# Kernel optimization log

Measured on AMD Instinct MI355X. Metric: run time of the kernel, lower is better.

Reference implementation:

```python
import jax, jax.numpy as jnp
import numpy as np

B, N_ATOM, N_TOK = 1, 1536, 384
C_ATOM, C_PAIR, C_TOK = 128, 16, 384
C_HID, H, L = 32, 4, 3
HID = 2 * C_ATOM  # n_transition = 2
N_QUERY, N_KEY, INF = 32, 128, 1e9


def _ln(x, gamma=None, beta=None, eps=1e-5):
    mu = jnp.mean(x, axis=-1, keepdims=True)
    var = jnp.mean(jnp.square(x - mu), axis=-1, keepdims=True)
    y = (x - mu) * jax.lax.rsqrt(var + eps)
    if gamma is not None:
        y = y * gamma
    if beta is not None:
        y = y + beta
    return y


def _adaln(a, s, gamma_s, Wg, bg, Ws):
    an = _ln(a)            # LN without affine
    sn = _ln(s, gamma_s)   # scale-only LN
    return jax.nn.sigmoid(sn @ Wg + bg) * an + sn @ Ws


def _block_mask():
    # AtomTransformer.forward: 32-query x 128-key block-local mask
    offset = N_QUERY // 2 - 0.5
    n_center = N_ATOM // N_QUERY + 1
    centers = offset + jnp.arange(n_center, dtype=jnp.float32) * N_QUERY
    idx = jnp.arange(N_ATOM, dtype=jnp.float32)[:, None]
    row = (jnp.abs(idx - centers[None, :]) < N_QUERY / 2).astype(jnp.float32)
    col = (jnp.abs(idx - centers[None, :]) < N_KEY / 2).astype(jnp.float32)
    return (row @ col.T - 1.0) * INF   # [N,N]: 0 in-window, -INF outside


def _forward(ref_pos, ref_mask, ref_element, ref_charge, ref_atom_name_chars,
             ref_space_uid, token_mask, atom_to_token_index,
             W_feats, W_ref_offset, W_inv_sq, W_valid, W_l, W_m,
             W_mlp1, W_mlp2, W_mlp3, W_out_tok,
             attn_ada_gamma_s, attn_ada_Wg, attn_ada_bg, attn_ada_Ws,
             Wq, bq, Wk, Wv, lnz_g, lnz_b, Wb, Wgate, Wo, Wsg, bsg,
             tr_ada_gamma_s, tr_ada_Wg, tr_ada_bg, tr_ada_Ws,
             tr_W1, tr_W2, tr_Wog, tr_bog, tr_Wout):
    # --- RefAtomFeatureEmbedder (AF3 Alg 5 lines 1-6) ---
    feats = jnp.concatenate([
        ref_pos, ref_mask[..., None], ref_element, ref_charge[..., None],
        ref_atom_name_chars.reshape(B, N_ATOM, -1), ref_space_uid[..., None]], axis=-1)
    cl = feats @ W_feats                                     # [B,N,C_ATOM]
    d = ref_pos[:, None, :, :] - ref_pos[:, :, None, :]      # d[l,m] = pos[m]-pos[l]
    v = (ref_space_uid[:, None, :] == ref_space_uid[:, :, None]).astype(jnp.float32)[..., None]
    plm = (d @ W_ref_offset) * v
    inv_sq = 1.0 / (1.0 + jnp.sum(d * d, axis=-1, keepdims=True))
    plm = plm + (inv_sq @ W_inv_sq) * v + (v @ W_valid) * v  # [B,N,N,C_PAIR]
    ql = cl
    # --- single -> pair conditioning + pair MLP ---
    crelu = jax.nn.relu(cl)
    plm = plm + (crelu @ W_l)[:, :, None, :] + (crelu @ W_m)[:, None, :, :]
    h = jax.nn.relu(plm) @ W_mlp1
    h = jax.nn.relu(h) @ W_mlp2
    h = jax.nn.relu(h) @ W_mlp3
    plm = plm + h
    # --- AtomTransformer (Alg 7) -> DiffusionTransformer (Alg 23) ---
    beta = _block_mask()                                     # [N,N]
    atom_mask = jnp.einsum('blt,bt->bl', atom_to_token_index, token_mask)
    mask_bias = (atom_mask - 1.0)[:, None, None, :] * INF    # [B,1,1,N]
    a, s = ql, cl
    inv_sqrt = 1.0 / np.sqrt(C_HID)
    for i in range(L):
        # AttentionPairBias (Alg 24)
        an = _adaln(a, s, attn_ada_gamma_s[i], attn_ada_Wg[i], attn_ada_bg[i], attn_ada_Ws[i])
        q = (an @ Wq[i] + bq[i]).reshape(B, N_ATOM, H, C_HID)
        k = (an @ Wk[i]).reshape(B, N_ATOM, H, C_HID)
        vv = (an @ Wv[i]).reshape(B, N_ATOM, H, C_HID)
        zb = _ln(plm, lnz_g[i], lnz_b[i]) @ Wb[i]            # [B,N,N,H]
        logits = (jnp.einsum('bqhc,bkhc->bhqk', q, k) * inv_sqrt
                  + jnp.moveaxis(zb, -1, 1) + beta[None, None] + mask_bias)
        A = jax.nn.softmax(logits, axis=-1)
        o = jnp.einsum('bhqk,bkhc->bqhc', A, vv)
        g = jax.nn.sigmoid(an @ Wgate[i]).reshape(B, N_ATOM, H, C_HID)
        o = (g * o).reshape(B, N_ATOM, H * C_HID) @ Wo[i]
        attn_out = jax.nn.sigmoid(s @ Wsg[i] + bsg[i]) * o
        # ConditionedTransitionBlock (Alg 25) on pre-attention a (Alg 23)
        tn = _adaln(a, s, tr_ada_gamma_s[i], tr_ada_Wg[i], tr_ada_bg[i], tr_ada_Ws[i])
        hh = jax.nn.silu(tn @ tr_W1[i]) * (tn @ tr_W2[i])
        tr_out = jax.nn.sigmoid(s @ tr_Wog[i] + tr_bog[i]) * (hh @ tr_Wout[i])
        a = attn_out + tr_out
    # --- mean-aggregate atoms -> tokens (Alg 5 line 15) ---
    al = jax.nn.relu(a @ W_out_tok)                          # [B,N,C_TOK]
    counts = jnp.maximum(jnp.sum(atom_to_token_index, axis=1), 1.0)
    a_tok = jnp.einsum('blt,blc->btc', atom_to_token_index, al) / counts[..., None]
    return a_tok


def setup_inputs() -> dict:
    key = jax.random.key(0)
    ks = iter(jax.random.split(key, 80))

    def nrm(shape, scale=0.02):
        return jax.random.normal(next(ks), shape, dtype=jnp.float32) * scale

    inp = {}
    inp['ref_pos'] = jax.random.normal(next(ks), (B, N_ATOM, 3), dtype=jnp.float32) * 3.0
    inp['ref_mask'] = jnp.ones((B, N_ATOM), jnp.float32)
    elem = jax.random.randint(next(ks), (B, N_ATOM), 0, 128)
    inp['ref_element'] = jax.nn.one_hot(elem, 128, dtype=jnp.float32)
    inp['ref_charge'] = jax.random.normal(next(ks), (B, N_ATOM), dtype=jnp.float32)
    chars = jax.random.randint(next(ks), (B, N_ATOM, 4), 0, 64)
    inp['ref_atom_name_chars'] = jax.nn.one_hot(chars, 64, dtype=jnp.float32)
    inp['ref_space_uid'] = jnp.broadcast_to(
        (jnp.arange(N_ATOM) // 8).astype(jnp.float32), (B, N_ATOM))
    inp['token_mask'] = jnp.ones((B, N_TOK), jnp.float32)
    tok = (jnp.arange(N_ATOM) * N_TOK) // N_ATOM  # ~4 atoms per token
    inp['atom_to_token_index'] = jnp.broadcast_to(
        jax.nn.one_hot(tok, N_TOK, dtype=jnp.float32), (B, N_ATOM, N_TOK))
    # embedder params
    inp['W_feats'] = nrm((390, C_ATOM))
    inp['W_ref_offset'] = nrm((3, C_PAIR))
    inp['W_inv_sq'] = nrm((1, C_PAIR))
    inp['W_valid'] = nrm((1, C_PAIR))
    inp['W_l'] = nrm((C_ATOM, C_PAIR))
    inp['W_m'] = nrm((C_ATOM, C_PAIR))
    inp['W_mlp1'] = nrm((C_PAIR, C_PAIR))
    inp['W_mlp2'] = nrm((C_PAIR, C_PAIR))
    inp['W_mlp3'] = nrm((C_PAIR, C_PAIR))
    inp['W_out_tok'] = nrm((C_ATOM, C_TOK))
    # DiffusionTransformer params, stacked over L blocks
    inp['attn_ada_gamma_s'] = jnp.ones((L, C_ATOM), jnp.float32)
    inp['attn_ada_Wg'] = nrm((L, C_ATOM, C_ATOM))
    inp['attn_ada_bg'] = jnp.zeros((L, C_ATOM), jnp.float32)
    inp['attn_ada_Ws'] = nrm((L, C_ATOM, C_ATOM))
    inp['Wq'] = nrm((L, C_ATOM, H * C_HID))
    inp['bq'] = jnp.zeros((L, H * C_HID), jnp.float32)
    inp['Wk'] = nrm((L, C_ATOM, H * C_HID))
    inp['Wv'] = nrm((L, C_ATOM, H * C_HID))
    inp['lnz_g'] = jnp.ones((L, C_PAIR), jnp.float32)
    inp['lnz_b'] = jnp.zeros((L, C_PAIR), jnp.float32)
    inp['Wb'] = nrm((L, C_PAIR, H))
    inp['Wgate'] = nrm((L, C_ATOM, H * C_HID))
    inp['Wo'] = nrm((L, H * C_HID, C_ATOM))
    inp['Wsg'] = nrm((L, C_ATOM, C_ATOM))
    inp['bsg'] = jnp.full((L, C_ATOM), -2.0, jnp.float32)
    inp['tr_ada_gamma_s'] = jnp.ones((L, C_ATOM), jnp.float32)
    inp['tr_ada_Wg'] = nrm((L, C_ATOM, C_ATOM))
    inp['tr_ada_bg'] = jnp.zeros((L, C_ATOM), jnp.float32)
    inp['tr_ada_Ws'] = nrm((L, C_ATOM, C_ATOM))
    inp['tr_W1'] = nrm((L, C_ATOM, HID))
    inp['tr_W2'] = nrm((L, C_ATOM, HID))
    inp['tr_Wog'] = nrm((L, C_ATOM, C_ATOM))
    inp['tr_bog'] = jnp.full((L, C_ATOM), -2.0, jnp.float32)
    inp['tr_Wout'] = nrm((L, HID, C_ATOM))
    return inp


def reference(ref_pos, ref_mask, ref_element, ref_charge, ref_atom_name_chars,
              ref_space_uid, token_mask, atom_to_token_index,
              W_feats, W_ref_offset, W_inv_sq, W_valid, W_l, W_m,
              W_mlp1, W_mlp2, W_mlp3, W_out_tok,
              attn_ada_gamma_s, attn_ada_Wg, attn_ada_bg, attn_ada_Ws,
              Wq, bq, Wk, Wv, lnz_g, lnz_b, Wb, Wgate, Wo, Wsg, bsg,
              tr_ada_gamma_s, tr_ada_Wg, tr_ada_bg, tr_ada_Ws,
              tr_W1, tr_W2, tr_Wog, tr_bog, tr_Wout):
    return _forward(ref_pos, ref_mask, ref_element, ref_charge, ref_atom_name_chars,
                    ref_space_uid, token_mask, atom_to_token_index,
                    W_feats, W_ref_offset, W_inv_sq, W_valid, W_l, W_m,
                    W_mlp1, W_mlp2, W_mlp3, W_out_tok,
                    attn_ada_gamma_s, attn_ada_Wg, attn_ada_bg, attn_ada_Ws,
                    Wq, bq, Wk, Wv, lnz_g, lnz_b, Wb, Wgate, Wo, Wsg, bsg,
                    tr_ada_gamma_s, tr_ada_Wg, tr_ada_bg, tr_ada_Ws,
                    tr_W1, tr_W2, tr_Wog, tr_bog, tr_Wout)
```

## Files before the change

### kernel.cpp

```cpp
#include <hip/hip_runtime.h>
#include <math.h>

#define N_ATOM 1536
#define NB     48
#define NLAYER 3
#define NC     196608L
#define ZSTRIDE 786432L

struct GD { const float* A; const float* B; float* C; const float* ks; const float* bias;
            int act; int ldb; int ldc; int _pad; };
struct GB { GD g[18]; };

__global__ __launch_bounds__(128) void embed_tok_kernel(
    const float* __restrict__ pos, const float* __restrict__ rmask,
    const float* __restrict__ elem, const float* __restrict__ charge,
    const float* __restrict__ chars, const float* __restrict__ uid,
    const float* __restrict__ Wf, const float* __restrict__ W_l, const float* __restrict__ W_m,
    const float* __restrict__ a2t, const float* __restrict__ tmask,
    float* __restrict__ cl, float* __restrict__ aa, float* __restrict__ clnorm,
    float* __restrict__ pl, float* __restrict__ pm,
    int* __restrict__ tok, float* __restrict__ counts, float* __restrict__ amask)
{
  int l = blockIdx.x, c = threadIdx.x;
  __shared__ int sidx[6];
  __shared__ float red[128];
  __shared__ float crow[128];
  if (elem[(long)l * 128 + c] > 0.5f) sidx[0] = c;
  float v0 = chars[(long)l * 256 + c];
  if (v0 > 0.5f) sidx[1 + (c >> 6)] = c & 63;
  float v1 = chars[(long)l * 256 + 128 + c];
  if (v1 > 0.5f) sidx[3 + (c >> 6)] = c & 63;
  for (int j = c; j < 384; j += 128)
    if (a2t[(long)l * 384 + j] > 0.5f) sidx[5] = j;
  __syncthreads();
  float acc = pos[l * 3 + 0] * Wf[c]
            + pos[l * 3 + 1] * Wf[128 + c]
            + pos[l * 3 + 2] * Wf[256 + c]
            + rmask[l] * Wf[384 + c]
            + Wf[(4 + sidx[0]) * 128 + c]
            + charge[l] * Wf[132 * 128 + c]
            + Wf[(133 + sidx[1]) * 128 + c]
            + Wf[(197 + sidx[2]) * 128 + c]
            + Wf[(261 + sidx[3]) * 128 + c]
            + Wf[(325 + sidx[4]) * 128 + c]
            + uid[l] * Wf[389 * 128 + c];
  long gi = (long)l * 128 + c;
  cl[gi] = acc; aa[gi] = acc; crow[c] = fmaxf(acc, 0.f);
  red[c] = acc; __syncthreads();
  for (int s = 64; s > 0; s >>= 1) { if (c < s) red[c] += red[c + s]; __syncthreads(); }
  float mu = red[0] * (1.f / 128.f); __syncthreads();
  float d = acc - mu; red[c] = d * d; __syncthreads();
  for (int s = 64; s > 0; s >>= 1) { if (c < s) red[c] += red[c + s]; __syncthreads(); }
  clnorm[gi] = d * rsqrtf(red[0] * (1.f / 128.f) + 1e-5f);
  if (c < 32) {
    const float* W = (c < 16) ? W_l : W_m;
    int o = c & 15;
    float s = 0.f;
    for (int cc = 0; cc < 128; cc++) s = fmaf(crow[cc], W[cc * 16 + o], s);
    if (c < 16) pl[l * 16 + o] = s; else pm[l * 16 + o] = s;
  }
  if (c == 127) {
    int j = sidx[5];
    tok[l] = j; amask[l] = tmask[j];
    atomicAdd(counts + j, 1.0f);
  }
}

__global__ __launch_bounds__(128) void adaln_kernel(
    const float* __restrict__ a,
    const float* __restrict__ sgA, const float* __restrict__ adA,
    const float* __restrict__ sgT, const float* __restrict__ adT,
    float* __restrict__ an, float* __restrict__ tn)
{
  __shared__ float red[128];
  int l = blockIdx.x, c = threadIdx.x;
  float x = a[(long)l * 128 + c];
  red[c] = x; __syncthreads();
  for (int s = 64; s > 0; s >>= 1) { if (c < s) red[c] += red[c + s]; __syncthreads(); }
  float mu = red[0] * (1.f / 128.f); __syncthreads();
  float d = x - mu; red[c] = d * d; __syncthreads();
  for (int s = 64; s > 0; s >>= 1) { if (c < s) red[c] += red[c + s]; __syncthreads(); }
  float nv = d * rsqrtf(red[0] * (1.f / 128.f) + 1e-5f);
  long i = (long)l * 128 + c;
  an[i] = sgA[i] * nv + adA[i];
  tn[i] = sgT[i] * nv + adT[i];
}

__device__ __forceinline__ void gemm64_body(float* sm, const float* A, const float* B, float* C,
                                            const float* ks, const float* bias, int act,
                                            int ldb, int ldc, int row0, int col0) {
  float* As = sm; float* Bs = sm + 2176;
  int tid = threadIdx.x;
  int tx = tid & 15, ty = tid >> 4;
  float acc[4][4] = {};
  for (int k0 = 0; k0 < 128; k0 += 32) {
    __syncthreads();
    { int r = tid >> 3, k4 = tid & 7;
#pragma unroll
      for (int half = 0; half < 2; half++) {
        int row = r + half * 32;
        float4 v = *(const float4*)(A + (long)(row0 + row) * 128 + k0 + k4 * 4);
        if (ks) { const float* kp = ks + k0 + k4 * 4; v.x *= kp[0]; v.y *= kp[1]; v.z *= kp[2]; v.w *= kp[3]; }
        As[(k4 * 4 + 0) * 68 + row] = v.x; As[(k4 * 4 + 1) * 68 + row] = v.y;
        As[(k4 * 4 + 2) * 68 + row] = v.z; As[(k4 * 4 + 3) * 68 + row] = v.w;
      } }
    { int kk = tid >> 4, n4 = tid & 15;
#pragma unroll
      for (int half = 0; half < 2; half++) {
        int k = kk + half * 16;
        *(float4*)&Bs[k * 68 + n4 * 4] = *(const float4*)(B + (long)(k0 + k) * ldb + col0 + n4 * 4);
      } }
    __syncthreads();
#pragma unroll
    for (int kk = 0; kk < 32; kk++) {
      float4 a = *(const float4*)&As[kk * 68 + ty * 4];
      float4 b = *(const float4*)&Bs[kk * 68 + tx * 4];
      float av[4] = {a.x, a.y, a.z, a.w}, bv[4] = {b.x, b.y, b.z, b.w};
#pragma unroll
      for (int i = 0; i < 4; i++)
#pragma unroll
        for (int j = 0; j < 4; j++) acc[i][j] = fmaf(av[i], bv[j], acc[i][j]);
    }
  }
  __syncthreads();
#pragma unroll
  for (int i = 0; i < 4; i++) {
    int row = row0 + ty * 4 + i;
#pragma unroll
    for (int j = 0; j < 4; j++) {
      int col = col0 + tx * 4 + j;
      float x = acc[i][j];
      if (bias) x += bias[col];
      if (act == 1) x = 1.f / (1.f + expf(-x));
      else if (act == 2) x = fmaxf(x, 0.f);
      C[(long)row * ldc + col] = x;
    }
  }
}

__global__ __launch_bounds__(256) void gemm64(GB args, int M)
{
  __shared__ float sm[4352];
  GD d = args.g[blockIdx.z];
  gemm64_body(sm, d.A, d.B, d.C, d.ks, d.bias, d.act, d.ldb, d.ldc, blockIdx.y * 64, blockIdx.x * 64);
}

__global__ __launch_bounds__(256) void zpre_kernel(
    const float* __restrict__ pos, const float* __restrict__ uid,
    const float* __restrict__ Wro, const float* __restrict__ Winv, const float* __restrict__ Wval,
    const float* __restrict__ M1, const float* __restrict__ M2, const float* __restrict__ M3,
    const float* __restrict__ Lg, const float* __restrict__ Lb, const float* __restrict__ Wb,
    const float* __restrict__ pl, const float* __restrict__ pm, float* __restrict__ zb,
    GB ba)
{
  __shared__ float sm[4352];
  int bid = blockIdx.x, tid = threadIdx.x;
  if (bid >= 768) {
    int u = bid - 768;
    GD d = ba.g[u / 48];
    int tt = u % 48;
    gemm64_body(sm, d.A, d.B, d.C, d.ks, d.bias, d.act, d.ldb, d.ldc, (tt >> 1) * 64, (tt & 1) * 64);
    return;
  }
  if (tid < 48)  sm[tid] = Wro[tid];
  if (tid < 16)  { sm[48 + tid] = Winv[tid]; sm[64 + tid] = Wval[tid]; }
  sm[80 + tid] = M1[tid]; sm[336 + tid] = M2[tid]; sm[592 + tid] = M3[tid];
  if (tid < 48)  { sm[848 + tid] = Lg[tid]; sm[896 + tid] = Lb[tid]; }
  if (tid < 192) sm[944 + tid] = Wb[tid];
  __syncthreads();
  const float* sWro = sm;      const float* sWinv = sm + 48;  const float* sWval = sm + 64;
  const float* sM1 = sm + 80;  const float* sM2 = sm + 336;   const float* sM3 = sm + 592;
  const float* sLg = sm + 848; const float* sLb = sm + 896;   const float* sWb = sm + 944;
  int b = bid >> 4;
  int pc = (bid & 15) * 256 + tid;
  int qi = pc >> 7, kj = pc & 127;
  int l = b * 32 + qi, m = b * 32 - 48 + kj;
  long base = ((long)(b * 32 + qi) * 128 + kj) * 4;
  if (m < 0 || m >= N_ATOM) {
    for (int i = 0; i < NLAYER; i++)
      for (int h = 0; h < 4; h++) zb[i * ZSTRIDE + base + h] = 0.f;
    return;
  }
  float dx = pos[m * 3 + 0] - pos[l * 3 + 0];
  float dy = pos[m * 3 + 1] - pos[l * 3 + 1];
  float dz = pos[m * 3 + 2] - pos[l * 3 + 2];
  float v = (uid[m] == uid[l]) ? 1.f : 0.f;
  float inv = 1.f / (1.f + dx * dx + dy * dy + dz * dz);
  float pv[16], ha[16], hb[16];
#pragma unroll
  for (int j = 0; j < 16; j++)
    pv[j] = v * (dx * sWro[j] + dy * sWro[16 + j] + dz * sWro[32 + j] + inv * sWinv[j] + sWval[j])
            + pl[l * 16 + j] + pm[m * 16 + j];
#pragma unroll
  for (int jo = 0; jo < 16; jo++) { float s = 0.f; for (int ji = 0; ji < 16; ji++) s = fmaf(fmaxf(pv[ji], 0.f), sM1[ji * 16 + jo], s); ha[jo] = s; }
#pragma unroll
  for (int jo = 0; jo < 16; jo++) { float s = 0.f; for (int ji = 0; ji < 16; ji++) s = fmaf(fmaxf(ha[ji], 0.f), sM2[ji * 16 + jo], s); hb[jo] = s; }
#pragma unroll
  for (int jo = 0; jo < 16; jo++) { float s = 0.f; for (int ji = 0; ji < 16; ji++) s = fmaf(fmaxf(hb[ji], 0.f), sM3[ji * 16 + jo], s); ha[jo] = s; }
#pragma unroll
  for (int j = 0; j < 16; j++) pv[j] += ha[j];
  for (int i = 0; i < NLAYER; i++) {
    float mu = 0.f;
#pragma unroll
    for (int j = 0; j < 16; j++) mu += pv[j];
    mu *= (1.f / 16.f);
    float var = 0.f;
#pragma unroll
    for (int j = 0; j < 16; j++) { float dd = pv[j] - mu; var += dd * dd; }
    var *= (1.f / 16.f);
    float rs = rsqrtf(var + 1e-5f);
    float zn[16];
#pragma unroll
    for (int j = 0; j < 16; j++) zn[j] = (pv[j] - mu) * rs * sLg[i * 16 + j] + sLb[i * 16 + j];
    for (int h = 0; h < 4; h++) {
      float s = 0.f;
#pragma unroll
      for (int j = 0; j < 16; j++) s = fmaf(zn[j], sWb[i * 64 + j * 4 + h], s);
      zb[i * ZSTRIDE + base + h] = s;
    }
  }
}

__global__ __launch_bounds__(256) void attn_kernel(
    const float* __restrict__ qb, const float* __restrict__ kb, const float* __restrict__ vb,
    const float* __restrict__ gb, const float* __restrict__ zb, const float* __restrict__ amask,
    float* __restrict__ go)
{
  __shared__ float qs[16][36], ks[128][36], vs[128][36], ps[16][132];
  int bx = blockIdx.x, h = blockIdx.y, t = threadIdx.x;
  int b = bx >> 1, half = bx & 1;
  int q0 = b * 32 + half * 16;
  int kbase = b * 32 - 48;
  if (t < 128) {
    int qi = t >> 3, c4 = t & 7;
    *(float4*)&qs[qi][c4 * 4] = *(const float4*)(qb + (long)(q0 + qi) * 128 + h * 32 + c4 * 4);
  }
  for (int idx = t; idx < 128 * 8; idx += 256) {
    int kj = idx >> 3, c4 = idx & 7;
    int m = kbase + kj;
    float4 kv = make_float4(0.f, 0.f, 0.f, 0.f), vv = make_float4(0.f, 0.f, 0.f, 0.f);
    if (m >= 0 && m < N_ATOM) {
      kv = *(const float4*)(kb + (long)m * 128 + h * 32 + c4 * 4);
      vv = *(const float4*)(vb + (long)m * 128 + h * 32 + c4 * 4);
    }
    *(float4*)&ks[kj][c4 * 4] = kv;
    *(float4*)&vs[kj][c4 * 4] = vv;
  }
  __syncthreads();
  const float isq = 0.17677669529663687f;
  for (int p = t; p < 2048; p += 256) {
    int qi = p >> 7, kj = p & 127;
    int m = kbase + kj;
    float s = 0.f;
#pragma unroll
    for (int c4 = 0; c4 < 8; c4++) {
      float4 a = *(const float4*)&qs[qi][c4 * 4];
      float4 k4 = *(const float4*)&ks[kj][c4 * 4];
      s = fmaf(a.x, k4.x, s); s = fmaf(a.y, k4.y, s);
      s = fmaf(a.z, k4.z, s); s = fmaf(a.w, k4.w, s);
    }
    float logit;
    if (m >= 0 && m < N_ATOM) {
      logit = s * isq + zb[(((long)(q0 + qi)) * 128 + kj) * 4 + h] + (amask[m] - 1.f) * 1e9f;
    } else {
      logit = -1e9f;
    }
    ps[qi][kj] = logit;
  }
  __syncthreads();
  {
    int row = t >> 4, ln = t & 15;
    float mx = -1e30f;
    for (int kj = ln; kj < 128; kj += 16) mx = fmaxf(mx, ps[row][kj]);
#pragma unroll
    for (int o = 8; o > 0; o >>= 1) mx = fmaxf(mx, __shfl_xor(mx, o));
    float sm = 0.f;
    for (int kj = ln; kj < 128; kj += 16) { float e = expf(ps[row][kj] - mx); ps[row][kj] = e; sm += e; }
#pragma unroll
    for (int o = 8; o > 0; o >>= 1) sm += __shfl_xor(sm, o);
    float r = 1.f / sm;
    for (int kj = ln; kj < 128; kj += 16) ps[row][kj] *= r;
  }
  __syncthreads();
  {
    int qi = t >> 4, seg = (t >> 3) & 1, c4 = t & 7;
    float4 acc = make_float4(0.f, 0.f, 0.f, 0.f);
    int kj0 = seg * 64;
#pragma unroll 4
    for (int kj = kj0; kj < kj0 + 64; kj++) {
      float p = ps[qi][kj];
      float4 v = *(const float4*)&vs[kj][c4 * 4];
      acc.x = fmaf(p, v.x, acc.x); acc.y = fmaf(p, v.y, acc.y);
      acc.z = fmaf(p, v.z, acc.z); acc.w = fmaf(p, v.w, acc.w);
    }
    acc.x += __shfl_xor(acc.x, 8);
    acc.y += __shfl_xor(acc.y, 8);
    acc.z += __shfl_xor(acc.z, 8);
    acc.w += __shfl_xor(acc.w, 8);
    if (seg == 0) {
      long gi = (long)(q0 + qi) * 128 + h * 32 + c4 * 4;
      float4 g = *(const float4*)(gb + gi);
      acc.x *= g.x; acc.y *= g.y; acc.z *= g.z; acc.w *= g.w;
      *(float4*)(go + gi) = acc;
    }
  }
}

__global__ __launch_bounds__(256) void gemm_dual32(
    const float* __restrict__ A1, const float* __restrict__ B1,
    const float* __restrict__ h1, const float* __restrict__ h2, const float* __restrict__ B2,
    const float* __restrict__ g1, const float* __restrict__ g2,
    float* __restrict__ C)
{
  __shared__ float As[32 * 36];
  __shared__ float Bs[32 * 68];
  const int N = 128;
  int t = threadIdx.x;
  int row0 = blockIdx.y * 32, col0 = blockIdx.x * 64;
  int tx = t & 15, ty = t >> 4;
  float acc1[2][4] = {}, acc2[2][4] = {};
  for (int k0 = 0; k0 < 128; k0 += 32) {
    __syncthreads();
    { int r = t >> 3, k4 = t & 7;
      float4 v = *(const float4*)(A1 + (long)(row0 + r) * 128 + k0 + k4 * 4);
      As[(k4 * 4 + 0) * 36 + r] = v.x; As[(k4 * 4 + 1) * 36 + r] = v.y;
      As[(k4 * 4 + 2) * 36 + r] = v.z; As[(k4 * 4 + 3) * 36 + r] = v.w;
    }
    for (int e = t; e < 512; e += 256) {
      int k = e >> 4, n4 = e & 15;
      *(float4*)&Bs[k * 68 + n4 * 4] = *(const float4*)(B1 + (long)(k0 + k) * N + col0 + n4 * 4);
    }
    __syncthreads();
#pragma unroll
    for (int kk = 0; kk < 32; kk++) {
      float a0 = As[kk * 36 + ty * 2], a1 = As[kk * 36 + ty * 2 + 1];
      float4 b = *(const float4*)&Bs[kk * 68 + tx * 4];
      float bv[4] = {b.x, b.y, b.z, b.w};
#pragma unroll
      for (int j = 0; j < 4; j++) {
        acc1[0][j] = fmaf(a0, bv[j], acc1[0][j]);
        acc1[1][j] = fmaf(a1, bv[j], acc1[1][j]);
      }
    }
  }
  for (int k0 = 0; k0 < 256; k0 += 32) {
    __syncthreads();
    { int r = t >> 3, k4 = t & 7;
      long o = (long)(row0 + r) * 256 + k0 + k4 * 4;
      float4 x = *(const float4*)(h1 + o);
      float4 y = *(const float4*)(h2 + o);
      As[(k4 * 4 + 0) * 36 + r] = (x.x / (1.f + expf(-x.x))) * y.x;
      As[(k4 * 4 + 1) * 36 + r] = (x.y / (1.f + expf(-x.y))) * y.y;
      As[(k4 * 4 + 2) * 36 + r] = (x.z / (1.f + expf(-x.z))) * y.z;
      As[(k4 * 4 + 3) * 36 + r] = (x.w / (1.f + expf(-x.w))) * y.w;
    }
    for (int e = t; e < 512; e += 256) {
      int k = e >> 4, n4 = e & 15;
      *(float4*)&Bs[k * 68 + n4 * 4] = *(const float4*)(B2 + (long)(k0 + k) * N + col0 + n4 * 4);
    }
    __syncthreads();
#pragma unroll
    for (int kk = 0; kk < 32; kk++) {
      float a0 = As[kk * 36 + ty * 2], a1 = As[kk * 36 + ty * 2 + 1];
      float4 b = *(const float4*)&Bs[kk * 68 + tx * 4];
      float bv[4] = {b.x, b.y, b.z, b.w};
#pragma unroll
      for (int j = 0; j < 4; j++) {
        acc2[0][j] = fmaf(a0, bv[j], acc2[0][j]);
        acc2[1][j] = fmaf(a1, bv[j], acc2[1][j]);
      }
    }
  }
#pragma unroll
  for (int i = 0; i < 2; i++) {
    long o = (long)(row0 + ty * 2 + i) * N + col0 + tx * 4;
    float4 ga = *(const float4*)(g1 + o);
    float4 gb = *(const float4*)(g2 + o);
    float4 r;
    r.x = ga.x * acc1[i][0] + gb.x * acc2[i][0];
    r.y = ga.y * acc1[i][1] + gb.y * acc2[i][1];
    r.z = ga.z * acc1[i][2] + gb.z * acc2[i][2];
    r.w = ga.w * acc1[i][3] + gb.w * acc2[i][3];
    *(float4*)(C + o) = r;
  }
}

__global__ __launch_bounds__(256) void gemm_scatter(
    const float* __restrict__ A, const float* __restrict__ B,
    const int* __restrict__ tok, const float* __restrict__ counts,
    float* __restrict__ out, int K)
{
  __shared__ float As[32][68];
  __shared__ float Bs[32][68];
  int tid = threadIdx.x;
  int row0 = blockIdx.y * 64, col0 = blockIdx.x * 64;
  int tx = tid & 15, ty = tid >> 4;
  float acc[4][4] = {};
  for (int k0 = 0; k0 < K; k0 += 32) {
    __syncthreads();
    { int r = tid >> 3, k4 = tid & 7;
#pragma unroll
      for (int half = 0; half < 2; half++) {
        int row = r + half * 32;
        float4 v = *(const float4*)(A + (long)(row0 + row) * K + k0 + k4 * 4);
        As[k4 * 4 + 0][row] = v.x; As[k4 * 4 + 1][row] = v.y;
        As[k4 * 4 + 2][row] = v.z; As[k4 * 4 + 3][row] = v.w;
      } }
    { int kk = tid >> 4, n4 = tid & 15;
#pragma unroll
      for (int half = 0; half < 2; half++) {
        int k = kk + half * 16;
        float4 v = *(const float4*)(B + (long)(k0 + k) * 384 + col0 + n4 * 4);
        *(float4*)&Bs[k][n4 * 4] = v;
      } }
    __syncthreads();
#pragma unroll
    for (int kk = 0; kk < 32; kk++) {
      float4 a = *(const float4*)&As[kk][ty * 4];
      float4 b = *(const float4*)&Bs[kk][tx * 4];
      float av[4] = {a.x, a.y, a.z, a.w}, bv[4] = {b.x, b.y, b.z, b.w};
#pragma unroll
      for (int i = 0; i < 4; i++)
#pragma unroll
        for (int j = 0; j < 4; j++) acc[i][j] = fmaf(av[i], bv[j], acc[i][j]);
    }
  }
  __syncthreads();
#pragma unroll
  for (int i = 0; i < 4; i++) {
    int row = row0 + ty * 4 + i;
    int tk = tok[row];
    float inv = 1.f / fmaxf(counts[tk], 1.f);
#pragma unroll
    for (int j = 0; j < 4; j++) {
      int col = col0 + tx * 4 + j;
      atomicAdd(&out[(long)tk * 384 + col], fmaxf(acc[i][j], 0.f) * inv);
    }
  }
}

extern "C" void kernel_launch(void* const* d_in, const int* in_sizes, int n_in,
                              void* d_out, int out_size, void* d_ws, size_t ws_size,
                              hipStream_t stream)
{
  const float* pos    = (const float*)d_in[0];
  const float* rmask  = (const float*)d_in[1];
  const float* elem   = (const float*)d_in[2];
  const float* charge = (const float*)d_in[3];
  const float* chars  = (const float*)d_in[4];
  const float* uid    = (const float*)d_in[5];
  const float* tmask  = (const float*)d_in[6];
  const float* a2t    = (const float*)d_in[7];
  const float* Wf     = (const float*)d_in[8];
  const float* Wro    = (const float*)d_in[9];
  const float* Winv   = (const float*)d_in[10];
  const float* Wval   = (const float*)d_in[11];
  const float* W_l    = (const float*)d_in[12];
  const float* W_m    = (const float*)d_in[13];
  const float* M1     = (const float*)d_in[14];
  const float* M2     = (const float*)d_in[15];
  const float* M3     = (const float*)d_in[16];
  const float* Wtok   = (const float*)d_in[17];
  const float* gA     = (const float*)d_in[18];
  const float* WgA    = (const float*)d_in[19];
  const float* bgA    = (const float*)d_in[20];
  const float* WsA    = (const float*)d_in[21];
  const float* Wq     = (const float*)d_in[22];
  const float* bq     = (const float*)d_in[23];
  const float* Wk     = (const float*)d_in[24];
  const float* Wv     = (const float*)d_in[25];
  const float* Lg     = (const float*)d_in[26];
  const float* Lb     = (const float*)d_in[27];
  const float* Wb     = (const float*)d_in[28];
  const float* Wgate  = (const float*)d_in[29];
  const float* Wo     = (const float*)d_in[30];
  const float* Wsg    = (const float*)d_in[31];
  const float* bsg    = (const float*)d_in[32];
  const float* gT     = (const float*)d_in[33];
  const float* WgT    = (const float*)d_in[34];
  const float* bgT    = (const float*)d_in[35];
  const float* WsT    = (const float*)d_in[36];
  const float* trW1   = (const float*)d_in[37];
  const float* trW2   = (const float*)d_in[38];
  const float* Wog    = (const float*)d_in[39];
  const float* bog    = (const float*)d_in[40];
  const float* Wout   = (const float*)d_in[41];
  float* out = (float*)d_out;

  float* ws = (float*)d_ws;
  size_t off = 0;
  auto alloc = [&](size_t n) { float* p = ws + off; off += n; return p; };
  float* cl     = alloc(NC);
  float* aa     = alloc(NC);
  float* clnorm = alloc(NC);
  float* an     = alloc(NC);
  float* tn     = alloc(NC);
  float* qbuf   = alloc(NC);
  float* kbuf   = alloc(NC);
  float* vbuf   = alloc(NC);
  float* gbuf   = alloc(NC);
  float* gobuf  = alloc(NC);
  float* h1     = alloc((size_t)N_ATOM * 256);
  float* h2     = alloc((size_t)N_ATOM * 256);
  float* pl     = alloc((size_t)N_ATOM * 16);
  float* pm     = alloc((size_t)N_ATOM * 16);
  float* zbias  = alloc((size_t)NLAYER * ZSTRIDE);
  float* sgA    = alloc(NC * NLAYER);
  float* adA    = alloc(NC * NLAYER);
  float* sgT    = alloc(NC * NLAYER);
  float* adT    = alloc(NC * NLAYER);
  float* gsg    = alloc(NC * NLAYER);
  float* gog    = alloc(NC * NLAYER);
  float* counts = alloc(384);
  float* amask  = alloc(N_ATOM);
  int*   tok    = (int*)alloc(N_ATOM);
  (void)ws_size; (void)in_sizes; (void)n_in; (void)out_size;

  (void)hipMemsetAsync(counts, 0, 384 * sizeof(float), stream);
  (void)hipMemsetAsync(out, 0, (size_t)384 * 384 * sizeof(float), stream);

  embed_tok_kernel<<<N_ATOM, 128, 0, stream>>>(pos, rmask, elem, charge, chars, uid, Wf,
                                               W_l, W_m, a2t, tmask,
                                               cl, aa, clnorm, pl, pm, tok, counts, amask);

  {
    GB ba = {};
    for (int i = 0; i < NLAYER; i++) {
      size_t o = (size_t)i * NC;
      ba.g[i * 6 + 0] = { clnorm, WgA + i * 16384, sgA + o, gA + i * 128, bgA + i * 128, 1, 128, 128, 0 };
      ba.g[i * 6 + 1] = { clnorm, WsA + i * 16384, adA + o, gA + i * 128, nullptr,       0, 128, 128, 0 };
      ba.g[i * 6 + 2] = { clnorm, WgT + i * 16384, sgT + o, gT + i * 128, bgT + i * 128, 1, 128, 128, 0 };
      ba.g[i * 6 + 3] = { clnorm, WsT + i * 16384, adT + o, gT + i * 128, nullptr,       0, 128, 128, 0 };
      ba.g[i * 6 + 4] = { cl,     Wsg + i * 16384, gsg + o, nullptr,      bsg + i * 128, 1, 128, 128, 0 };
      ba.g[i * 6 + 5] = { cl,     Wog + i * 16384, gog + o, nullptr,      bog + i * 128, 1, 128, 128, 0 };
    }
    zpre_kernel<<<768 + 864, 256, 0, stream>>>(pos, uid, Wro, Winv, Wval, M1, M2, M3,
                                               Lg, Lb, Wb, pl, pm, zbias, ba);
  }

  for (int i = 0; i < NLAYER; i++) {
    size_t o = (size_t)i * NC;
    adaln_kernel<<<N_ATOM, 128, 0, stream>>>(aa, sgA + o, adA + o, sgT + o, adT + o, an, tn);
    {
      GB ba = {};
      ba.g[0] = { an, Wq + i * 16384,        qbuf, nullptr, bq + i * 128, 0, 128, 128, 0 };
      ba.g[1] = { an, Wk + i * 16384,        kbuf, nullptr, nullptr,      0, 128, 128, 0 };
      ba.g[2] = { an, Wv + i * 16384,        vbuf, nullptr, nullptr,      0, 128, 128, 0 };
      ba.g[3] = { an, Wgate + i * 16384,     gbuf, nullptr, nullptr,      1, 128, 128, 0 };
      ba.g[4] = { tn, trW1 + i * 32768,       h1,  nullptr, nullptr,      0, 256, 256, 0 };
      ba.g[5] = { tn, trW1 + i * 32768 + 128, h1 + 128, nullptr, nullptr, 0, 256, 256, 0 };
      ba.g[6] = { tn, trW2 + i * 32768,       h2,  nullptr, nullptr,      0, 256, 256, 0 };
      ba.g[7] = { tn, trW2 + i * 32768 + 128, h2 + 128, nullptr, nullptr, 0, 256, 256, 0 };
      gemm64<<<dim3(2, 24, 8), 256, 0, stream>>>(ba, N_ATOM);
    }
    attn_kernel<<<dim3(96, 4), 256, 0, stream>>>(qbuf, kbuf, vbuf, gbuf,
                                                 zbias + (size_t)i * ZSTRIDE, amask, gobuf);
    gemm_dual32<<<dim3(2, 48), 256, 0, stream>>>(gobuf, Wo + i * 16384, h1, h2, Wout + i * 32768,
                                                 gsg + o, gog + o, aa);
  }

  gemm_scatter<<<dim3(6, 24), 256, 0, stream>>>(aa, Wtok, tok, counts, out, 128);
}
```

Before: 351.5 us.

## Fuse next layer's AdaLN into output dual-GEMM epilogue with full-row tiles

The output dual GEMM is retiled so each block owns 16 full 128-wide rows. Its epilogue can then compute the LayerNorm statistics with warp shuffles and write the next layer's AdaLN outputs (an, tn) directly. This removes the per-layer adaln_kernel launches after the first, and for intermediate layers skips writing and re-reading the activation buffer. The trade-off is that each block loads the whole B tile and does more epilogue work, and LN variance now uses the E[x²]−μ² form instead of a two-pass computation.

```diff
diff --git a/kernel.cpp b/kernel.cpp
--- a/kernel.cpp
+++ b/kernel.cpp
@@ -306,83 +306,109 @@
   }
 }
 
-__global__ __launch_bounds__(256) void gemm_dual32(
+__global__ __launch_bounds__(256) void gemm_dual16(
     const float* __restrict__ A1, const float* __restrict__ B1,
     const float* __restrict__ h1, const float* __restrict__ h2, const float* __restrict__ B2,
-    const float* __restrict__ g1, const float* __restrict__ g2,
-    float* __restrict__ C)
-{
-  __shared__ float As[32 * 36];
-  __shared__ float Bs[32 * 68];
-  const int N = 128;
+    const float* __restrict__ g1, const float* __restrict__ g2, float* __restrict__ C,
+    const float* __restrict__ sg1, const float* __restrict__ ad1,
+    const float* __restrict__ sg2, const float* __restrict__ ad2,
+    float* __restrict__ an, float* __restrict__ tn)
+{
+  __shared__ float As[32 * 20];
+  __shared__ float Bs[32 * 132];
   int t = threadIdx.x;
-  int row0 = blockIdx.y * 32, col0 = blockIdx.x * 64;
-  int tx = t & 15, ty = t >> 4;
-  float acc1[2][4] = {}, acc2[2][4] = {};
+  int row0 = blockIdx.x * 16;
+  int r = t >> 4, cs = t & 15;
+  int cA = cs * 4, cB = 64 + cs * 4;
+  float a1a[4] = {}, a1b[4] = {}, a2a[4] = {}, a2b[4] = {};
   for (int k0 = 0; k0 < 128; k0 += 32) {
     __syncthreads();
-    { int r = t >> 3, k4 = t & 7;
-      float4 v = *(const float4*)(A1 + (long)(row0 + r) * 128 + k0 + k4 * 4);
-      As[(k4 * 4 + 0) * 36 + r] = v.x; As[(k4 * 4 + 1) * 36 + r] = v.y;
-      As[(k4 * 4 + 2) * 36 + r] = v.z; As[(k4 * 4 + 3) * 36 + r] = v.w;
-    }
-    for (int e = t; e < 512; e += 256) {
-      int k = e >> 4, n4 = e & 15;
-      *(float4*)&Bs[k * 68 + n4 * 4] = *(const float4*)(B1 + (long)(k0 + k) * N + col0 + n4 * 4);
+    if (t < 128) {
+      int row = t >> 3, k4 = t & 7;
+      float4 v = *(const float4*)(A1 + (long)(row0 + row) * 128 + k0 + k4 * 4);
+      As[(k4 * 4 + 0) * 20 + row] = v.x; As[(k4 * 4 + 1) * 20 + row] = v.y;
+      As[(k4 * 4 + 2) * 20 + row] = v.z; As[(k4 * 4 + 3) * 20 + row] = v.w;
+    }
+    for (int e = t; e < 1024; e += 256) {
+      int kk = e >> 5, c4 = e & 31;
+      *(float4*)&Bs[kk * 132 + c4 * 4] = *(const float4*)(B1 + (long)(k0 + kk) * 128 + c4 * 4);
     }
     __syncthreads();
 #pragma unroll
     for (int kk = 0; kk < 32; kk++) {
-      float a0 = As[kk * 36 + ty * 2], a1 = As[kk * 36 + ty * 2 + 1];
-      float4 b = *(const float4*)&Bs[kk * 68 + tx * 4];
-      float bv[4] = {b.x, b.y, b.z, b.w};
-#pragma unroll
-      for (int j = 0; j < 4; j++) {
-        acc1[0][j] = fmaf(a0, bv[j], acc1[0][j]);
-        acc1[1][j] = fmaf(a1, bv[j], acc1[1][j]);
-      }
+      float a = As[kk * 20 + r];
+      float4 b0 = *(const float4*)&Bs[kk * 132 + cA];
+      float4 b1 = *(const float4*)&Bs[kk * 132 + cB];
+      a1a[0] = fmaf(a, b0.x, a1a[0]); a1a[1] = fmaf(a, b0.y, a1a[1]);
+      a1a[2] = fmaf(a, b0.z, a1a[2]); a1a[3] = fmaf(a, b0.w, a1a[3]);
+      a1b[0] = fmaf(a, b1.x, a1b[0]); a1b[1] = fmaf(a, b1.y, a1b[1]);
+      a1b[2] = fmaf(a, b1.z, a1b[2]); a1b[3] = fmaf(a, b1.w, a1b[3]);
     }
   }
   for (int k0 = 0; k0 < 256; k0 += 32) {
     __syncthreads();
-    { int r = t >> 3, k4 = t & 7;
-      long o = (long)(row0 + r) * 256 + k0 + k4 * 4;
+    if (t < 128) {
+      int row = t >> 3, k4 = t & 7;
+      long o = (long)(row0 + row) * 256 + k0 + k4 * 4;
       float4 x = *(const float4*)(h1 + o);
       float4 y = *(const float4*)(h2 + o);
-      As[(k4 * 4 + 0) * 36 + r] = (x.x / (1.f + expf(-x.x))) * y.x;
-      As[(k4 * 4 + 1) * 36 + r] = (x.y / (1.f + expf(-x.y))) * y.y;
-      As[(k4 * 4 + 2) * 36 + r] = (x.z / (1.f + expf(-x.z))) * y.z;
-      As[(k4 * 4 + 3) * 36 + r] = (x.w / (1.f + expf(-x.w))) * y.w;
-    }
-    for (int e = t; e < 512; e += 256) {
-      int k = e >> 4, n4 = e & 15;
-      *(float4*)&Bs[k * 68 + n4 * 4] = *(const float4*)(B2 + (long)(k0 + k) * N + col0 + n4 * 4);
+      As[(k4 * 4 + 0) * 20 + row] = (x.x / (1.f + expf(-x.x))) * y.x;
+      As[(k4 * 4 + 1) * 20 + row] = (x.y / (1.f + expf(-x.y))) * y.y;
+      As[(k4 * 4 + 2) * 20 + row] = (x.z / (1.f + expf(-x.z))) * y.z;
+      As[(k4 * 4 + 3) * 20 + row] = (x.w / (1.f + expf(-x.w))) * y.w;
+    }
+    for (int e = t; e < 1024; e += 256) {
+      int kk = e >> 5, c4 = e & 31;
+      *(float4*)&Bs[kk * 132 + c4 * 4] = *(const float4*)(B2 + (long)(k0 + kk) * 128 + c4 * 4);
     }
     __syncthreads();
 #pragma unroll
     for (int kk = 0; kk < 32; kk++) {
-      float a0 = As[kk * 36 + ty * 2], a1 = As[kk * 36 + ty * 2 + 1];
-      float4 b = *(const float4*)&Bs[kk * 68 + tx * 4];
-      float bv[4] = {b.x, b.y, b.z, b.w};
-#pragma unroll
-      for (int j = 0; j < 4; j++) {
-        acc2[0][j] = fmaf(a0, bv[j], acc2[0][j]);
-        acc2[1][j] = fmaf(a1, bv[j], acc2[1][j]);
-      }
-    }
-  }
-#pragma unroll
-  for (int i = 0; i < 2; i++) {
-    long o = (long)(row0 + ty * 2 + i) * N + col0 + tx * 4;
-    float4 ga = *(const float4*)(g1 + o);
-    float4 gb = *(const float4*)(g2 + o);
-    float4 r;
-    r.x = ga.x * acc1[i][0] + gb.x * acc2[i][0];
-    r.y = ga.y * acc1[i][1] + gb.y * acc2[i][1];
-    r.z = ga.z * acc1[i][2] + gb.z * acc2[i][2];
-    r.w = ga.w * acc1[i][3] + gb.w * acc2[i][3];
-    *(float4*)(C + o) = r;
-  }
+      float a = As[kk * 20 + r];
+      float4 b0 = *(const float4*)&Bs[kk * 132 + cA];
+      float4 b1 = *(const float4*)&Bs[kk * 132 + cB];
+      a2a[0] = fmaf(a, b0.x, a2a[0]); a2a[1] = fmaf(a, b0.y, a2a[1]);
+      a2a[2] = fmaf(a, b0.z, a2a[2]); a2a[3] = fmaf(a, b0.w, a2a[3]);
+      a2b[0] = fmaf(a, b1.x, a2b[0]); a2b[1] = fmaf(a, b1.y, a2b[1]);
+      a2b[2] = fmaf(a, b1.z, a2b[2]); a2b[3] = fmaf(a, b1.w, a2b[3]);
+    }
+  }
+  int row = row0 + r;
+  long oA = (long)row * 128 + cA, oB = (long)row * 128 + cB;
+  float4 g1a = *(const float4*)(g1 + oA), g1b = *(const float4*)(g1 + oB);
+  float4 g2a = *(const float4*)(g2 + oA), g2b = *(const float4*)(g2 + oB);
+  float xa[4], xb[4];
+  xa[0] = g1a.x * a1a[0] + g2a.x * a2a[0]; xa[1] = g1a.y * a1a[1] + g2a.y * a2a[1];
+  xa[2] = g1a.z * a1a[2] + g2a.z * a2a[2]; xa[3] = g1a.w * a1a[3] + g2a.w * a2a[3];
+  xb[0] = g1b.x * a1b[0] + g2b.x * a2b[0]; xb[1] = g1b.y * a1b[1] + g2b.y * a2b[1];
+  xb[2] = g1b.z * a1b[2] + g2b.z * a2b[2]; xb[3] = g1b.w * a1b[3] + g2b.w * a2b[3];
+  if (sg1 == nullptr) {
+    *(float4*)(C + oA) = make_float4(xa[0], xa[1], xa[2], xa[3]);
+    *(float4*)(C + oB) = make_float4(xb[0], xb[1], xb[2], xb[3]);
+    return;
+  }
+  float s = 0.f, s2 = 0.f;
+#pragma unroll
+  for (int j = 0; j < 4; j++) { s += xa[j] + xb[j]; s2 = fmaf(xa[j], xa[j], s2); s2 = fmaf(xb[j], xb[j], s2); }
+#pragma unroll
+  for (int o = 8; o > 0; o >>= 1) { s += __shfl_xor(s, o); s2 += __shfl_xor(s2, o); }
+  float mu = s * (1.f / 128.f);
+  float rsd = rsqrtf(fmaxf(s2 * (1.f / 128.f) - mu * mu, 0.f) + 1e-5f);
+  float4 sA1 = *(const float4*)(sg1 + oA), sB1 = *(const float4*)(sg1 + oB);
+  float4 aA1 = *(const float4*)(ad1 + oA), aB1 = *(const float4*)(ad1 + oB);
+  float4 sA2 = *(const float4*)(sg2 + oA), sB2 = *(const float4*)(sg2 + oB);
+  float4 aA2 = *(const float4*)(ad2 + oA), aB2 = *(const float4*)(ad2 + oB);
+  float na[4], nb[4];
+#pragma unroll
+  for (int j = 0; j < 4; j++) { na[j] = (xa[j] - mu) * rsd; nb[j] = (xb[j] - mu) * rsd; }
+  *(float4*)(an + oA) = make_float4(sA1.x * na[0] + aA1.x, sA1.y * na[1] + aA1.y,
+                                    sA1.z * na[2] + aA1.z, sA1.w * na[3] + aA1.w);
+  *(float4*)(an + oB) = make_float4(sB1.x * nb[0] + aB1.x, sB1.y * nb[1] + aB1.y,
+                                    sB1.z * nb[2] + aB1.z, sB1.w * nb[3] + aB1.w);
+  *(float4*)(tn + oA) = make_float4(sA2.x * na[0] + aA2.x, sA2.y * na[1] + aA2.y,
+                                    sA2.z * na[2] + aA2.z, sA2.w * na[3] + aA2.w);
+  *(float4*)(tn + oB) = make_float4(sB2.x * nb[0] + aB2.x, sB2.y * nb[1] + aB2.y,
+                                    sB2.z * nb[2] + aB2.z, sB2.w * nb[3] + aB2.w);
 }
 
 __global__ __launch_bounds__(256) void gemm_scatter(
@@ -538,9 +564,9 @@
                                                Lg, Lb, Wb, pl, pm, zbias, ba);
   }
 
+  adaln_kernel<<<N_ATOM, 128, 0, stream>>>(aa, sgA, adA, sgT, adT, an, tn);
+
   for (int i = 0; i < NLAYER; i++) {
-    size_t o = (size_t)i * NC;
-    adaln_kernel<<<N_ATOM, 128, 0, stream>>>(aa, sgA + o, adA + o, sgT + o, adT + o, an, tn);
     {
       GB ba = {};
       ba.g[0] = { an, Wq + i * 16384,        qbuf, nullptr, bq + i * 128, 0, 128, 128, 0 };
@@ -555,8 +581,17 @@
     }
     attn_kernel<<<dim3(96, 4), 256, 0, stream>>>(qbuf, kbuf, vbuf, gbuf,
                                                  zbias + (size_t)i * ZSTRIDE, amask, gobuf);
-    gemm_dual32<<<dim3(2, 48), 256, 0, stream>>>(gobuf, Wo + i * 16384, h1, h2, Wout + i * 32768,
-                                                 gsg + o, gog + o, aa);
+    size_t o = (size_t)i * NC;
+    if (i < NLAYER - 1) {
+      size_t o1 = (size_t)(i + 1) * NC;
+      gemm_dual16<<<96, 256, 0, stream>>>(gobuf, Wo + i * 16384, h1, h2, Wout + i * 32768,
+                                          gsg + o, gog + o, aa,
+                                          sgA + o1, adA + o1, sgT + o1, adT + o1, an, tn);
+    } else {
+      gemm_dual16<<<96, 256, 0, stream>>>(gobuf, Wo + i * 16384, h1, h2, Wout + i * 32768,
+                                          gsg + o, gog + o, aa,
+                                          nullptr, nullptr, nullptr, nullptr, an, tn);
+    }
   }
 
   gemm_scatter<<<dim3(6, 24), 256, 0, stream>>>(aa, Wtok, tok, counts, out, 128);
```

After: 368.1 us. 1.05x slower.
